# Optimization experiments

Measured on AMD Instinct MI355X. Metric: run time of the kernel, lower is better.

The kernel has to match this reference:

```python
import jax, jax.numpy as jnp
import numpy as np


def setup_inputs() -> dict:
    key = jax.random.key(0)
    k1, k2, k3 = jax.random.split(key, 3)
    B, C, H, W = 2, 32, 128, 256
    maxdisp = 12
    feat_l = jax.random.normal(k1, (B, C, H, W), dtype=jnp.float32)
    feat_r = jax.random.normal(k2, (B, C, H, W), dtype=jnp.float32)
    # disparity estimate in pixels at this feature scale
    disp = jax.random.uniform(k3, (B, 1, H, W), dtype=jnp.float32) * 64.0
    return {"feat_l": feat_l, "feat_r": feat_r, "disp": disp, "maxdisp": maxdisp}


def _warp_1d(feat_r, d_map):
    """Warp feat_r [B,C,H,W] horizontally by d_map [B,H,W].

    Equivalent to torch grid_sample(bilinear, zeros padding, align_corners=True)
    with grid x = xx - d, y = yy: y lands exactly on pixel centers, so the
    bilinear interp degenerates to 1-D interp along W with zero padding.
    """
    B, C, H, W = feat_r.shape
    xx = jnp.arange(W, dtype=feat_r.dtype)
    px = xx[None, None, :] - d_map  # [B,H,W] sampling x-coordinate
    x0 = jnp.floor(px)
    w1 = px - x0                     # weight of right neighbor
    w0 = 1.0 - w1
    x0i = x0.astype(jnp.int32)
    x1i = x0i + 1
    m0 = ((x0i >= 0) & (x0i <= W - 1)).astype(feat_r.dtype)  # zeros padding
    m1 = ((x1i >= 0) & (x1i <= W - 1)).astype(feat_r.dtype)

    def gather(idx):
        idxc = jnp.clip(idx, 0, W - 1)[:, None, :, :]  # [B,1,H,W]
        return jnp.take_along_axis(feat_r, jnp.broadcast_to(idxc, (B, C, H, W)), axis=3)

    g0 = gather(x0i)
    g1 = gather(x1i)
    return g0 * (w0 * m0)[:, None] + g1 * (w1 * m1)[:, None]  # [B,C,H,W]


def reference(feat_l, feat_r, disp, maxdisp):
    B, C, H, W = feat_l.shape
    D = 2 * maxdisp - 1
    shifts = jnp.arange(-maxdisp + 1, maxdisp, dtype=feat_l.dtype)  # [D]
    # batch_disp - batch_shift, laid out [D,B,H,W] (plane-major for vmap)
    d_all = disp[:, 0][None, :, :, :] - shifts[:, None, None, None]  # [D,B,H,W]
    warped = jax.vmap(lambda d: _warp_1d(feat_r, d))(d_all)          # [D,B,C,H,W]
    # L1 norm over channels of (feat_l - warped)
    cost = jnp.sum(jnp.abs(feat_l[None] - warped), axis=2)           # [D,B,H,W]
    return jnp.transpose(cost, (1, 0, 2, 3))                         # [B,D,H,W]
```

## Files before the change

kernel.cpp:

```cpp
#include <hip/hip_runtime.h>

#define BB 2
#define CC 32
#define HH 128
#define WW 256
#define MAXD 12
#define DD (2 * MAXD - 1)

#define PADL 80
#define SROW (PADL + WW + 16)

__global__ __launch_bounds__(WW) void cost_volume_kernel(
    const float* __restrict__ feat_l,
    const float* __restrict__ feat_r,
    const float* __restrict__ disp,
    float* __restrict__ out)
{
    __shared__ float smem[CC * SROW];

    const int w  = threadIdx.x;
    const int bh = blockIdx.x;
    const int b  = bh / HH;
    const int h  = bh % HH;

    for (int i = threadIdx.x; i < CC * SROW; i += WW) smem[i] = 0.0f;
    __syncthreads();

    for (int c = 0; c < CC; ++c) {
        smem[c * SROW + PADL + w] =
            feat_r[(((size_t)b * CC + c) * HH + h) * WW + w];
    }
    __syncthreads();

    const float d    = disp[((size_t)b * HH + h) * WW + w];
    const float base = (float)w - d;
    const float x0f  = floorf(base);
    const float w1   = base - x0f;
    const float w0   = 1.0f - w1;
    int x0b = (int)x0f;
    x0b = min(max(x0b, -(PADL - (MAXD - 1))), WW - 1);
    const int sbase = PADL + x0b - (MAXD - 1);

    float acc[DD];
#pragma unroll
    for (int di = 0; di < DD; ++di) acc[di] = 0.0f;

    for (int c = 0; c < CC; ++c) {
        const float flv = feat_l[(((size_t)b * CC + c) * HH + h) * WW + w];
        const float* sp = &smem[c * SROW + sbase];
        float rv[DD + 1];
#pragma unroll
        for (int j = 0; j <= DD; ++j) rv[j] = sp[j];
#pragma unroll
        for (int di = 0; di < DD; ++di) {
            const float v = w0 * rv[di] + w1 * rv[di + 1];
            acc[di] += fabsf(flv - v);
        }
    }

#pragma unroll
    for (int di = 0; di < DD; ++di) {
        out[(((size_t)b * DD + di) * HH + h) * WW + w] = acc[di];
    }
}

extern "C" void kernel_launch(void* const* d_in, const int* in_sizes, int n_in,
                              void* d_out, int out_size, void* d_ws, size_t ws_size,
                              hipStream_t stream)
{
    const float* feat_l = (const float*)d_in[0];
    const float* feat_r = (const float*)d_in[1];
    const float* disp   = (const float*)d_in[2];
    float* out = (float*)d_out;

    dim3 grid(BB * HH);
    dim3 block(WW);
    cost_volume_kernel<<<grid, block, 0, stream>>>(feat_l, feat_r, disp, out);
}
```

Before: 82.57 us.

## Split disparities across blocks and store feat_r channel-interleaved in shared memory

The grid is split three ways along the disparity axis, so each block computes 8 of the 23 disparity planes. The shared-memory copy of feat_r is transposed to a column-major layout with channels contiguous, padded to a stride of 36. This allows float4 LDS reads and a sliding pair of columns reused across adjacent disparities, and it drops the zero-fill pass by masking out-of-range columns during the load. The cost is that each block reloads feat_r and feat_l for the row, so global traffic rises, and the last group wastes one of its eight disparities.

New measurement: 120.8 us. +46.3%, slower.

```diff
diff --git a/kernel.cpp b/kernel.cpp
--- a/kernel.cpp
+++ b/kernel.cpp
@@ -6,61 +6,114 @@
 #define WW 256
 #define MAXD 12
 #define DD (2 * MAXD - 1)
+#define NG 3
+#define GSZ 8
+#define NC 328
+#define SC 36
+#define HW (HH * WW)
 
-#define PADL 80
-#define SROW (PADL + WW + 16)
 
-__global__ __launch_bounds__(WW) void cost_volume_kernel(
+__global__ __launch_bounds__(256, 3) void cost_volume_kernel(
     const float* __restrict__ feat_l,
     const float* __restrict__ feat_r,
     const float* __restrict__ disp,
     float* __restrict__ out)
 {
-    __shared__ float smem[CC * SROW];
+    __shared__ __align__(16) float smem[NC * SC];
 
-    const int w  = threadIdx.x;
-    const int bh = blockIdx.x;
-    const int b  = bh / HH;
-    const int h  = bh % HH;
+    const int t  = threadIdx.x;
+    const int g  = blockIdx.x >> 8;
+    const int bh = blockIdx.x & 255;
+    const int b  = bh >> 7;
+    const int h  = bh & 127;
+    const int COL0 = 8 * g - 75;
 
-    for (int i = threadIdx.x; i < CC * SROW; i += WW) smem[i] = 0.0f;
-    __syncthreads();
-
-    for (int c = 0; c < CC; ++c) {
-        smem[c * SROW + PADL + w] =
-            feat_r[(((size_t)b * CC + c) * HH + h) * WW + w];
+    {
+        const int colLane = t & 63;
+        const int q0 = t >> 6;
+        #pragma unroll
+        for (int cc = 0; cc < 6; ++cc) {
+            const int col = cc * 64 + colLane;
+            if (col < NC) {
+                const int gcol = col + COL0;
+                const bool inr = (gcol >= 0) && (gcol < WW);
+                const int gc = min(max(gcol, 0), WW - 1);
+                #pragma unroll
+                for (int qq = 0; qq < 2; ++qq) {
+                    const int q = q0 + 4 * qq;
+                    const size_t base =
+                        ((size_t)(b * CC + 4 * q)) * HW + (size_t)h * WW + gc;
+                    const float x0 = feat_r[base];
+                    const float x1 = feat_r[base + HW];
+                    const float x2 = feat_r[base + 2 * HW];
+                    const float x3 = feat_r[base + 3 * HW];
+                    float4 v;
+                    v.x = inr ? x0 : 0.0f;
+                    v.y = inr ? x1 : 0.0f;
+                    v.z = inr ? x2 : 0.0f;
+                    v.w = inr ? x3 : 0.0f;
+                    *(float4*)&smem[col * SC + 4 * q] = v;
+                }
+            }
+        }
     }
     __syncthreads();
 
-    const float d    = disp[((size_t)b * HH + h) * WW + w];
-    const float base = (float)w - d;
-    const float x0f  = floorf(base);
-    const float w1   = base - x0f;
+    const float d    = disp[(size_t)bh * WW + t];
+    const float px   = (float)t - d;
+    const float x0f  = floorf(px);
+    const float w1   = px - x0f;
     const float w0   = 1.0f - w1;
     int x0b = (int)x0f;
-    x0b = min(max(x0b, -(PADL - (MAXD - 1))), WW - 1);
-    const int sbase = PADL + x0b - (MAXD - 1);
+    x0b = min(max(x0b, -64), WW - 1);
+    const int lb = x0b + 64;
 
-    float acc[DD];
-#pragma unroll
-    for (int di = 0; di < DD; ++di) acc[di] = 0.0f;
+    float acc[GSZ];
+    #pragma unroll
+    for (int j = 0; j < GSZ; ++j) acc[j] = 0.0f;
 
-    for (int c = 0; c < CC; ++c) {
-        const float flv = feat_l[(((size_t)b * CC + c) * HH + h) * WW + w];
-        const float* sp = &smem[c * SROW + sbase];
-        float rv[DD + 1];
-#pragma unroll
-        for (int j = 0; j <= DD; ++j) rv[j] = sp[j];
-#pragma unroll
-        for (int di = 0; di < DD; ++di) {
-            const float v = w0 * rv[di] + w1 * rv[di + 1];
-            acc[di] += fabsf(flv - v);
+    #pragma unroll
+    for (int half = 0; half < 2; ++half) {
+        const int c0 = half * 16;
+
+        float fl[16];
+        #pragma unroll
+        for (int k = 0; k < 16; ++k)
+            fl[k] = feat_l[((size_t)(b * CC + c0 + k)) * HW + (size_t)h * WW + t];
+
+        auto loadcol = [&](int j, float4* dst) {
+            const float* cp = &smem[(lb + j) * SC + c0];
+            #pragma unroll
+            for (int k = 0; k < 4; ++k) dst[k] = *(const float4*)(cp + 4 * k);
+        };
+        auto dotstep = [&](const float4* Ca, const float4* Cb) -> float {
+            float s0 = 0.0f, s1 = 0.0f;
+            #pragma unroll
+            for (int k = 0; k < 4; ++k) {
+                s0 += fabsf(fmaf(w1, Cb[k].x, fmaf(w0, Ca[k].x, -fl[4*k+0])));
+                s1 += fabsf(fmaf(w1, Cb[k].y, fmaf(w0, Ca[k].y, -fl[4*k+1])));
+                s0 += fabsf(fmaf(w1, Cb[k].z, fmaf(w0, Ca[k].z, -fl[4*k+2])));
+                s1 += fabsf(fmaf(w1, Cb[k].w, fmaf(w0, Ca[k].w, -fl[4*k+3])));
+            }
+            return s0 + s1;
+        };
+
+        float4 A[4], Bv[4];
+        loadcol(0, A);
+        #pragma unroll
+        for (int jj = 0; jj < 4; ++jj) {
+            loadcol(2 * jj + 1, Bv);
+            acc[2 * jj]     += dotstep(A, Bv);
+            loadcol(2 * jj + 2, A);
+            acc[2 * jj + 1] += dotstep(Bv, A);
         }
     }
 
-#pragma unroll
-    for (int di = 0; di < DD; ++di) {
-        out[(((size_t)b * DD + di) * HH + h) * WW + w] = acc[di];
+    #pragma unroll
+    for (int j = 0; j < GSZ; ++j) {
+        const int di = g * GSZ + j;
+        if (di < DD)
+            out[((size_t)(b * DD + di)) * HW + (size_t)h * WW + t] = acc[j];
     }
 }
 
@@ -73,7 +126,7 @@
     const float* disp   = (const float*)d_in[2];
     float* out = (float*)d_out;
 
-    dim3 grid(BB * HH);
-    dim3 block(WW);
+    dim3 grid(NG * BB * HH);
+    dim3 block(256);
     cost_volume_kernel<<<grid, block, 0, stream>>>(feat_l, feat_r, disp, out);
 }
```

## Split rows into segments with channel-split threads and float4 channel-interleaved LDS

Applied to the files above, without the earlier changes.

Each block now handles a 64-pixel segment of a row, and its four thread groups each own 8 channels. Right features are staged in LDS in a column-major, channel-interleaved layout so each tap is read as two float4s, and the taps rotate through a register window. The per-group partial sums over disparities are then combined through LDS. This gives four times more blocks for better occupancy, fewer scalar LDS reads and fewer registers per thread, at the cost of an extra LDS reduction pass and redundant halo loads per segment.

Result: faster. 78.01 us (median of 2 runs) (-5.5%).

```diff
diff --git a/kernel.cpp b/kernel.cpp
--- a/kernel.cpp
+++ b/kernel.cpp
@@ -4,63 +4,117 @@
 #define CC 32
 #define HH 128
 #define WW 256
-#define MAXD 12
-#define DD (2 * MAXD - 1)
+#define DD 23
+#define HW (HH * WW)
 
-#define PADL 80
-#define SROW (PADL + WW + 16)
+#define SEG 64
+#define NSEG 4
+#define NCOLS 151
+#define SC 36
+#define RED 23
 
-__global__ __launch_bounds__(WW) void cost_volume_kernel(
+
+__global__ __launch_bounds__(256, 4) void cost_volume_kernel(
     const float* __restrict__ feat_l,
     const float* __restrict__ feat_r,
     const float* __restrict__ disp,
     float* __restrict__ out)
 {
-    __shared__ float smem[CC * SROW];
+    __shared__ __align__(16) float smem[NCOLS * SC];
 
-    const int w  = threadIdx.x;
-    const int bh = blockIdx.x;
-    const int b  = bh / HH;
-    const int h  = bh % HH;
+    const int t  = threadIdx.x;
+    const int q  = t >> 6;
+    const int px = t & 63;
+    const int s  = blockIdx.x >> 8;
+    const int bh = blockIdx.x & 255;
+    const int b  = bh >> 7;
+    const int h  = bh & 127;
+    const int w  = s * SEG + px;
+    const int COL0 = s * SEG - 75;
+    const int c0 = q * 8;
 
-    for (int i = threadIdx.x; i < CC * SROW; i += WW) smem[i] = 0.0f;
-    __syncthreads();
+    float fl[8];
+    const size_t lbase = ((size_t)(b * CC + c0)) * HW + (size_t)h * WW + w;
+    #pragma unroll
+    for (int k = 0; k < 8; ++k) fl[k] = feat_l[lbase + (size_t)k * HW];
+    const float d = disp[(size_t)bh * WW + w];
 
-    for (int c = 0; c < CC; ++c) {
-        smem[c * SROW + PADL + w] =
-            feat_r[(((size_t)b * CC + c) * HH + h) * WW + w];
+    #pragma unroll
+    for (int cc = 0; cc < 3; ++cc) {
+        const int col = cc * 64 + px;
+        if (col < NCOLS) {
+            const int  gcol = col + COL0;
+            const bool inr  = (gcol >= 0) && (gcol < WW);
+            const int  gc   = min(max(gcol, 0), WW - 1);
+            #pragma unroll
+            for (int qq = 0; qq < 2; ++qq) {
+                const int cq = (q + 4 * qq) * 4;
+                const size_t base = ((size_t)(b * CC + cq)) * HW + (size_t)h * WW + gc;
+                const float x0 = feat_r[base];
+                const float x1 = feat_r[base + HW];
+                const float x2 = feat_r[base + 2 * HW];
+                const float x3 = feat_r[base + 3 * HW];
+                float4 v;
+                v.x = inr ? x0 : 0.0f;
+                v.y = inr ? x1 : 0.0f;
+                v.z = inr ? x2 : 0.0f;
+                v.w = inr ? x3 : 0.0f;
+                *(float4*)&smem[col * SC + cq] = v;
+            }
+        }
     }
     __syncthreads();
 
-    const float d    = disp[((size_t)b * HH + h) * WW + w];
-    const float base = (float)w - d;
-    const float x0f  = floorf(base);
-    const float w1   = base - x0f;
-    const float w0   = 1.0f - w1;
-    int x0b = (int)x0f;
-    x0b = min(max(x0b, -(PADL - (MAXD - 1))), WW - 1);
-    const int sbase = PADL + x0b - (MAXD - 1);
+    const float pxf = (float)w - d;
+    const float x0f = floorf(pxf);
+    const float w1  = pxf - x0f;
+    const float w0  = 1.0f - w1;
+    int lb = (int)x0f - COL0 - 11;
+    lb = min(max(lb, 0), NCOLS - 24);
+
+    float4 Ta[3], Tb[3];
+    #define LOADTAP(idx, j) { \
+        const float4* p_ = (const float4*)&smem[(lb + (j)) * SC + c0]; \
+        Ta[idx] = p_[0]; Tb[idx] = p_[1]; }
+
+    LOADTAP(0, 0)
+    LOADTAP(1, 1)
 
     float acc[DD];
-#pragma unroll
-    for (int di = 0; di < DD; ++di) acc[di] = 0.0f;
+    #pragma unroll
+    for (int di = 0; di < DD; ++di) {
+        if (di + 2 < 24) LOADTAP((di + 2) % 3, di + 2)
+        const float4 A0 = Ta[di % 3],       A1 = Tb[di % 3];
+        const float4 B0 = Ta[(di + 1) % 3], B1 = Tb[(di + 1) % 3];
+        float sA = 0.0f, sB = 0.0f;
+        sA += fabsf(fmaf(w0, A0.x, fmaf(w1, B0.x, -fl[0])));
+        sB += fabsf(fmaf(w0, A0.y, fmaf(w1, B0.y, -fl[1])));
+        sA += fabsf(fmaf(w0, A0.z, fmaf(w1, B0.z, -fl[2])));
+        sB += fabsf(fmaf(w0, A0.w, fmaf(w1, B0.w, -fl[3])));
+        sA += fabsf(fmaf(w0, A1.x, fmaf(w1, B1.x, -fl[4])));
+        sB += fabsf(fmaf(w0, A1.y, fmaf(w1, B1.y, -fl[5])));
+        sA += fabsf(fmaf(w0, A1.z, fmaf(w1, B1.z, -fl[6])));
+        sB += fabsf(fmaf(w0, A1.w, fmaf(w1, B1.w, -fl[7])));
+        acc[di] = sA + sB;
+    }
+    #undef LOADTAP
 
-    for (int c = 0; c < CC; ++c) {
-        const float flv = feat_l[(((size_t)b * CC + c) * HH + h) * WW + w];
-        const float* sp = &smem[c * SROW + sbase];
-        float rv[DD + 1];
-#pragma unroll
-        for (int j = 0; j <= DD; ++j) rv[j] = sp[j];
-#pragma unroll
+    __syncthreads();
+    if (q != 0) {
+        float* r = &smem[(q - 1) * (64 * RED) + px * RED];
+        #pragma unroll
+        for (int di = 0; di < DD; ++di) r[di] = acc[di];
+    }
+    __syncthreads();
+    if (q == 0) {
+        const float* r0 = &smem[0 * (64 * RED) + px * RED];
+        const float* r1 = &smem[1 * (64 * RED) + px * RED];
+        const float* r2 = &smem[2 * (64 * RED) + px * RED];
+        #pragma unroll
         for (int di = 0; di < DD; ++di) {
-            const float v = w0 * rv[di] + w1 * rv[di + 1];
-            acc[di] += fabsf(flv - v);
+            const float v = acc[di] + r0[di] + r1[di] + r2[di];
+            out[((size_t)(b * DD + di)) * HW + (size_t)h * WW + w] = v;
         }
-    }
-
-#pragma unroll
-    for (int di = 0; di < DD; ++di) {
-        out[(((size_t)b * DD + di) * HH + h) * WW + w] = acc[di];
     }
 }
 
@@ -73,7 +127,7 @@
     const float* disp   = (const float*)d_in[2];
     float* out = (float*)d_out;
 
-    dim3 grid(BB * HH);
-    dim3 block(WW);
+    dim3 grid(NSEG * BB * HH);
+    dim3 block(256);
     cost_volume_kernel<<<grid, block, 0, stream>>>(feat_l, feat_r, disp, out);
 }
```
